# Kernel optimization log

Measured on AMD Instinct MI355X. Metric: run time of the kernel, lower is better.

Reference implementation:

```python
import jax, jax.numpy as jnp
import numpy as np

HID, H, D, DFF = 128, 4, 128, 2048   # hidden_dim, nheads, out_feats per head, dim_feedforward
N, E, B = 32768, 524288, 32
EPS = 1e-5
SLOPE = 0.2  # DGL EdgeGATConv negative_slope default


def setup_inputs() -> dict:
    key = jax.random.key(0)
    ks = jax.random.split(key, 16)
    s = 0.05
    return {
        "h": jax.random.normal(ks[0], (N, HID), jnp.float32),
        "e": jax.random.normal(ks[1], (E, 1), jnp.float32),
        "src": jax.random.randint(ks[2], (E,), 0, N, jnp.int32),
        "dst": jax.random.randint(ks[3], (E,), 0, N, jnp.int32),
        "batch_size": B,
        # EdgeGATConv params (fc / fc_edge / res_fc are bias-free in DGL)
        "W_fc": jax.random.normal(ks[4], (HID, H * D), jnp.float32) * s,
        "attn_l": jax.random.normal(ks[5], (H, D), jnp.float32) * s,
        "attn_r": jax.random.normal(ks[6], (H, D), jnp.float32) * s,
        "W_fe": jax.random.normal(ks[7], (1, H * D), jnp.float32) * s,
        "attn_e": jax.random.normal(ks[8], (H, D), jnp.float32) * s,
        "W_res": jax.random.normal(ks[9], (HID, H * D), jnp.float32) * s,
        "gat_bias": jnp.zeros((H * D,), jnp.float32),
        # linear_mha + norms + FFN
        "W_mha": jax.random.normal(ks[10], (H * D, HID), jnp.float32) * s,
        "b_mha": jnp.zeros((HID,), jnp.float32),
        "n1_g": jnp.ones((HID,), jnp.float32),
        "n1_b": jnp.zeros((HID,), jnp.float32),
        "n2_g": jnp.ones((HID,), jnp.float32),
        "n2_b": jnp.zeros((HID,), jnp.float32),
        "W1": jax.random.normal(ks[11], (HID, DFF), jnp.float32) * s,
        "b1": jnp.zeros((DFF,), jnp.float32),
        "W2": jax.random.normal(ks[12], (DFF, HID), jnp.float32) * s,
        "b2": jnp.zeros((HID,), jnp.float32),
    }


def _ln(x, g, b):
    mu = x.mean(-1, keepdims=True)
    var = ((x - mu) ** 2).mean(-1, keepdims=True)
    return (x - mu) * jax.lax.rsqrt(var + EPS) * g + b


def reference(h, e, src, dst, batch_size, W_fc, attn_l, attn_r, W_fe, attn_e,
              W_res, gat_bias, W_mha, b_mha, n1_g, n1_b, n2_g, n2_b,
              W1, b1, W2, b2):
    n = h.shape[0]
    h0 = h
    # --- EdgeGATConv (eval mode: dropouts are identity) ---
    ft = (h @ W_fc).reshape(n, H, D)                         # (N,H,D)
    el = jnp.einsum("nhd,hd->nh", ft, attn_l)                # (N,H)
    er = jnp.einsum("nhd,hd->nh", ft, attn_r)
    fe = (e @ W_fe).reshape(-1, H, D)                        # (E,H,D)
    ee = jnp.einsum("ehd,hd->eh", fe, attn_e)                # (E,H)
    sc = jax.nn.leaky_relu(el[src] + er[dst] + ee, SLOPE)    # (E,H)
    # segment softmax over incoming edges of each dst node
    m = jax.ops.segment_max(sc, dst, num_segments=n)         # (N,H)
    m = jnp.where(jnp.isfinite(m), m, 0.0)                   # empty segments
    w = jnp.exp(sc - m[dst])
    z = jax.ops.segment_sum(w, dst, num_segments=n)
    zd = z[dst]
    alpha = w / jnp.where(zd == 0, 1.0, zd)                  # (E,H)
    msg = ft[src] * alpha[:, :, None]                        # (E,H,D)
    rst = jax.ops.segment_sum(msg, dst, num_segments=n)      # (N,H,D)
    rst = rst + (h0 @ W_res).reshape(n, H, D) + gat_bias.reshape(1, H, D)
    # --- transformer wrapper ---
    x = jax.nn.relu(rst).reshape(n, H * D)
    x = jax.nn.relu(x @ W_mha + b_mha)
    x = _ln(h0 + x, n1_g, n1_b)
    x = x.reshape(batch_size, -1, x.shape[1])                # (B, N/B, HID)
    ff = jax.nn.relu(x @ W1 + b1) @ W2 + b2
    return _ln(x + ff, n2_g, n2_b)
```

## Files before the change

### kernel.cpp

```cpp
#include <hip/hip_runtime.h>
#include <hip/hip_bf16.h>
#include <hip/hip_fp16.h>

#define N_NODES 32768
#define E_EDGES 524288
#define HIDDIM 128
#define FDIM 512
#define DFF 2048
#define LN_EPS 1e-5f
#define SLOPE 0.2f
#define CAP 64

typedef __bf16 bf16_t;
typedef __bf16 bf16x8 __attribute__((ext_vector_type(8)));
typedef float f32x4 __attribute__((ext_vector_type(4)));
typedef float f32x2 __attribute__((ext_vector_type(2)));

#define GLD_LDS16(gp, lp) __builtin_amdgcn_global_load_lds( \
    (const __attribute__((address_space(1))) unsigned int*)(gp), \
    (__attribute__((address_space(3))) unsigned int*)(lp), 16, 0, 0)

__device__ inline unsigned char f32_to_e4m3(float v) {
#if __has_builtin(__builtin_amdgcn_cvt_pk_fp8_f32)
    return (unsigned char)(__builtin_amdgcn_cvt_pk_fp8_f32(v, v, 0, false) & 0xff);
#else
    unsigned bits = __float_as_uint(v);
    unsigned sign = (bits >> 24) & 0x80;
    float av = fabsf(v);
    if (av >= 448.f) return (unsigned char)(sign | 0x7E);
    int e = (int)((bits >> 23) & 0xFF) - 127;
    if (e < -6) { int n = (int)rintf(av * 512.f); return (unsigned char)(sign | n); }
    float ulp = exp2f((float)(e - 3));
    int n = (int)rintf(av / ulp);
    if (n == 16) { e += 1; n = 8; }
    return (unsigned char)(sign | ((e + 7) << 3) | (n - 8));
#endif
}
template<bool HI>
__device__ inline f32x2 e4m3x2_to_f32(unsigned u) {
#if __has_builtin(__builtin_amdgcn_cvt_pk_f32_fp8)
    return __builtin_amdgcn_cvt_pk_f32_fp8(u, HI);
#else
    f32x2 r;
    unsigned b0 = HI ? ((u >> 16) & 0xff) : (u & 0xff);
    unsigned b1 = HI ? ((u >> 24) & 0xff) : ((u >> 8) & 0xff);
    unsigned bs[2] = {b0, b1};
    for (int i = 0; i < 2; ++i) {
        unsigned b = bs[i];
        float s = (b & 0x80) ? -1.f : 1.f;
        int e = (b >> 3) & 15, m = b & 7;
        float v = e ? (8 + m) * exp2f((float)(e - 10)) : m * exp2f(-9.f);
        r[i] = s * v;
    }
    return r;
#endif
}

__device__ inline void pack_range(const float* __restrict__ B, bf16_t* __restrict__ out,
                                  int id, int N) {
    const int g = id / N, n = id % N;
    union { bf16_t b[8]; uint4 u; } pk;
#pragma unroll
    for (int j = 0; j < 8; ++j) pk.b[j] = (bf16_t)B[(size_t)(g * 8 + j) * N + n];
    *(uint4*)(out + (size_t)id * 8) = pk.u;
}

__global__ __launch_bounds__(256) void prep_kernel(const float* __restrict__ h, bf16_t* __restrict__ hb,
                                                   const float* __restrict__ W_fc, bf16_t* __restrict__ Wfc_p,
                                                   const float* __restrict__ W_res, bf16_t* __restrict__ Wres_p,
                                                   const float* __restrict__ W_mha, bf16_t* __restrict__ Wmha_p,
                                                   const float* __restrict__ W1, bf16_t* __restrict__ W1_p,
                                                   const float* __restrict__ W2, bf16_t* __restrict__ W2_p,
                                                   const float* __restrict__ W_fe, const float* __restrict__ attn_e,
                                                   float* __restrict__ ce) {
    int bid = blockIdx.x;
    const int tid = threadIdx.x;
    if (bid < 4096) {
        const int id = bid * 256 + tid;
        const float4 v = ((const float4*)h)[id];
        union { bf16_t b[4]; uint2 u; } pk;
        pk.b[0] = (bf16_t)v.x; pk.b[1] = (bf16_t)v.y; pk.b[2] = (bf16_t)v.z; pk.b[3] = (bf16_t)v.w;
        *(uint2*)(hb + (size_t)id * 4) = pk.u;
        return;
    }
    bid -= 4096;
    if (bid < 32)  { pack_range(W_fc,  Wfc_p,  bid * 256 + tid, 512);  return; }
    bid -= 32;
    if (bid < 32)  { pack_range(W_res, Wres_p, bid * 256 + tid, 512);  return; }
    bid -= 32;
    if (bid < 32)  { pack_range(W_mha, Wmha_p, bid * 256 + tid, 128);  return; }
    bid -= 32;
    if (bid < 128) { pack_range(W1,    W1_p,   bid * 256 + tid, 2048); return; }
    bid -= 128;
    if (bid < 128) { pack_range(W2,    W2_p,   bid * 256 + tid, 128);  return; }
    if (tid < 128) {
        const float4 w = ((const float4*)W_fe)[tid];
        const float4 a = ((const float4*)attn_e)[tid];
        float p = w.x * a.x + w.y * a.y + w.z * a.z + w.w * a.w;
        for (int off = 16; off; off >>= 1) p += __shfl_down(p, off, 32);
        if ((tid & 31) == 0) ce[tid >> 5] = p;
    }
}

__global__ __launch_bounds__(256, 2) void gemm_ftres(const bf16_t* __restrict__ A,
                                                     const bf16_t* __restrict__ Bf,
                                                     const bf16_t* __restrict__ Brs,
                                                     const float* __restrict__ attn_l,
                                                     const float* __restrict__ attn_r,
                                                     unsigned char* __restrict__ ft8,
                                                     float* __restrict__ el,
                                                     float* __restrict__ er,
                                                     bf16_t* __restrict__ res) {
    __shared__ __align__(16) bf16_t lA[4096];
    __shared__ __align__(16) bf16_t lBf[4096];
    __shared__ __align__(16) bf16_t lBr[4096];
    __shared__ float s_el[2][128], s_er[2][128];
    const int tid = threadIdx.x, lane = tid & 63, wave = tid >> 6;
    const int wm = (wave >> 1) * 64, wn = (wave & 1) * 64;
    const int row0 = blockIdx.y * 128;
    const int head = blockIdx.x, col0 = head * 128;
    const int ko = lane >> 4, rl = lane & 15;
    f32x4 accf[4][4] = {};
    f32x4 accr[4][4] = {};
    const int c0 = tid, c1 = tid + 256;
    const int g0 = c0 >> 7, m0 = c0 & 127;
    const int g1 = c1 >> 7, m1 = c1 & 127;
    for (int k0 = 0; k0 < 128; k0 += 32) {
        __syncthreads();
        GLD_LDS16(A + (size_t)(row0 + m0) * 128 + k0 + g0 * 8, lA + c0 * 8);
        GLD_LDS16(A + (size_t)(row0 + m1) * 128 + k0 + g1 * 8, lA + c1 * 8);
        GLD_LDS16(Bf + ((size_t)(k0 / 8 + g0) * 512 + col0 + m0) * 8, lBf + c0 * 8);
        GLD_LDS16(Bf + ((size_t)(k0 / 8 + g1) * 512 + col0 + m1) * 8, lBf + c1 * 8);
        GLD_LDS16(Brs + ((size_t)(k0 / 8 + g0) * 512 + col0 + m0) * 8, lBr + c0 * 8);
        GLD_LDS16(Brs + ((size_t)(k0 / 8 + g1) * 512 + col0 + m1) * 8, lBr + c1 * 8);
        __syncthreads();
        bf16x8 af[4], bff[4], bfr[4];
#pragma unroll
        for (int i = 0; i < 4; ++i) {
            af[i]  = *(const bf16x8*)&lA[(ko * 128 + wm + i * 16 + rl) * 8];
            bff[i] = *(const bf16x8*)&lBf[(ko * 128 + wn + i * 16 + rl) * 8];
            bfr[i] = *(const bf16x8*)&lBr[(ko * 128 + wn + i * 16 + rl) * 8];
        }
#pragma unroll
        for (int i = 0; i < 4; ++i)
#pragma unroll
            for (int j = 0; j < 4; ++j) {
                accf[i][j] = __builtin_amdgcn_mfma_f32_16x16x32_bf16(af[i], bff[j], accf[i][j], 0, 0, 0);
                accr[i][j] = __builtin_amdgcn_mfma_f32_16x16x32_bf16(af[i], bfr[j], accr[i][j], 0, 0, 0);
            }
    }
    const int cr = (lane >> 4) * 4, cc = lane & 15;
    float al[4], ar[4];
#pragma unroll
    for (int j = 0; j < 4; ++j) {
        al[j] = attn_l[col0 + wn + j * 16 + cc];
        ar[j] = attn_r[col0 + wn + j * 16 + cc];
    }
#pragma unroll
    for (int i = 0; i < 4; ++i)
#pragma unroll
        for (int r = 0; r < 4; ++r) {
            const int row = row0 + wm + i * 16 + cr + r;
            float pel = 0.f, per = 0.f;
#pragma unroll
            for (int j = 0; j < 4; ++j) {
                const int col = col0 + wn + j * 16 + cc;
                const float v = accf[i][j][r];
                ft8[(size_t)row * 512 + col] = f32_to_e4m3(v);
                res[(size_t)row * 512 + col] = (bf16_t)accr[i][j][r];
                pel += v * al[j];
                per += v * ar[j];
            }
#pragma unroll
            for (int m = 1; m < 16; m <<= 1) {
                pel += __shfl_xor(pel, m);
                per += __shfl_xor(per, m);
            }
            if (cc == 0) {
                s_el[wn >> 6][wm + i * 16 + cr + r] = pel;
                s_er[wn >> 6][wm + i * 16 + cr + r] = per;
            }
        }
    __syncthreads();
    if (tid < 128) {
        el[(size_t)(row0 + tid) * 4 + head] = s_el[0][tid] + s_el[1][tid];
        er[(size_t)(row0 + tid) * 4 + head] = s_er[0][tid] + s_er[1][tid];
    }
}

__global__ __launch_bounds__(512, 2) void ffn_mega(const bf16_t* __restrict__ x1,
                                                   const bf16_t* __restrict__ Wm,
                                                   const float* __restrict__ b_mha,
                                                   const float* __restrict__ h0,
                                                   const float* __restrict__ n1g,
                                                   const float* __restrict__ n1b,
                                                   bf16_t* __restrict__ x3stash,
                                                   const bf16_t* __restrict__ W1p,
                                                   const float* __restrict__ b1,
                                                   const bf16_t* __restrict__ W2p,
                                                   const float* __restrict__ b2,
                                                   const float* __restrict__ gamma,
                                                   const float* __restrict__ beta,
                                                   float* __restrict__ out) {
    __shared__ __align__(16) bf16_t lW1[3][8192];
    __shared__ __align__(16) bf16_t lW2[4][8192];
    __shared__ __align__(16) bf16_t lY[2][8192];
    __shared__ float s_s1[2][128], s_s2[2][128], s_mu[128], s_rs[128];
    const int tid = threadIdx.x, lane = tid & 63, wave = tid >> 6;
    const int kh  = wave & 1;
    const int ds  = wave & 3;
    const int cg  = (wave >> 1) & 1;
    const int rg  = wave >> 2;
    const int wr  = rg * 64;
    const int wc1 = ds * 16;
    const int wc2 = cg * 64;
    const int row0 = blockIdx.x * 128;
    const int ko = lane >> 4, rl = lane & 15;
    const int cr = ko * 4, cc = rl;

    {
        const int rg2 = wave >> 1;
        const int cg2 = wave & 1;
        bf16_t* lA = &lY[0][0];
        bf16_t* lB = &lY[0][4096];
        f32x4 am[2][4] = {};
        for (int k0 = 0; k0 < 512; k0 += 32) {
            __syncthreads();
            {
                const int g = tid >> 7, m = tid & 127;
                GLD_LDS16(x1 + (size_t)(row0 + m) * 512 + k0 + g * 8, lA + tid * 8);
                GLD_LDS16(Wm + ((size_t)(k0 / 8 + g) * 128 + m) * 8, lB + tid * 8);
            }
            __syncthreads();
            bf16x8 af[2], bf[4];
#pragma unroll
            for (int i = 0; i < 2; ++i)
                af[i] = *(const bf16x8*)&lA[(ko * 128 + rg2 * 32 + i * 16 + rl) * 8];
#pragma unroll
            for (int j = 0; j < 4; ++j)
                bf[j] = *(const bf16x8*)&lB[(ko * 128 + cg2 * 64 + j * 16 + rl) * 8];
#pragma unroll
            for (int i = 0; i < 2; ++i)
#pragma unroll
                for (int j = 0; j < 4; ++j)
                    am[i][j] = __builtin_amdgcn_mfma_f32_16x16x32_bf16(af[i], bf[j], am[i][j], 0, 0, 0);
        }
#pragma unroll
        for (int j = 0; j < 4; ++j) {
            const int col = cg2 * 64 + j * 16 + cc;
            const float bb = b_mha[col];
#pragma unroll
            for (int i = 0; i < 2; ++i)
#pragma unroll
                for (int r = 0; r < 4; ++r) {
                    const int row = row0 + rg2 * 32 + i * 16 + cr + r;
                    am[i][j][r] = fmaxf(am[i][j][r] + bb, 0.f) + h0[(size_t)row * 128 + col];
                }
        }
#pragma unroll
        for (int i = 0; i < 2; ++i)
#pragma unroll
            for (int r = 0; r < 4; ++r) {
                float s1 = 0.f, s2 = 0.f;
#pragma unroll
                for (int j = 0; j < 4; ++j) { const float v = am[i][j][r]; s1 += v; s2 += v * v; }
#pragma unroll
                for (int m = 1; m < 16; m <<= 1) {
                    s1 += __shfl_xor(s1, m);
                    s2 += __shfl_xor(s2, m);
                }
                if (cc == 0) {
                    s_s1[cg2][rg2 * 32 + i * 16 + cr + r] = s1;
                    s_s2[cg2][rg2 * 32 + i * 16 + cr + r] = s2;
                }
            }
        __syncthreads();
        if (tid < 128) {
            const float a = s_s1[0][tid] + s_s1[1][tid];
            const float q = s_s2[0][tid] + s_s2[1][tid];
            const float mu = a * (1.f / 128.f);
            s_mu[tid] = mu;
            s_rs[tid] = rsqrtf(q * (1.f / 128.f) - mu * mu + LN_EPS);
        }
        __syncthreads();
        bf16_t* lX0 = &lW1[0][0];
#pragma unroll
        for (int j = 0; j < 4; ++j) {
            const int col = cg2 * 64 + j * 16 + cc;
            const float gg = n1g[col], bbta = n1b[col];
#pragma unroll
            for (int i = 0; i < 2; ++i)
#pragma unroll
                for (int r = 0; r < 4; ++r) {
                    const int rloc = rg2 * 32 + i * 16 + cr + r;
                    const bf16_t v = (bf16_t)((am[i][j][r] - s_mu[rloc]) * s_rs[rloc] * gg + bbta);
                    lX0[((col >> 3) * 128 + rloc) * 8 + (col & 7)] = v;
                    x3stash[(size_t)(row0 + rloc) * 128 + col] = v;
                }
        }
    }
    __syncthreads();

    bf16_t* lX = &lW1[0][0];
    bf16x8 afx[4][4];
#pragma unroll
    for (int ir = 0; ir < 4; ++ir)
#pragma unroll
        for (int kk = 0; kk < 4; ++kk)
            afx[ir][kk] = *(const bf16x8*)&lX[((kk * 4 + ko) * 128 + wr + ir * 16 + rl) * 8];
    asm volatile("s_waitcnt lgkmcnt(0)" ::: "memory");
    __builtin_amdgcn_s_barrier();
    __builtin_amdgcn_sched_barrier(0);

    auto stage_chunk = [&](int chn, bf16_t* w1d, bf16_t* w2d) {
#pragma unroll
        for (int it = 0; it < 2; ++it) {
            const int c = it * 512 + tid, g = c >> 6, n = c & 63;
            GLD_LDS16(W1p + ((size_t)g * 2048 + chn * 64 + n) * 8, w1d + c * 8);
        }
#pragma unroll
        for (int it = 0; it < 2; ++it) {
            const int c = it * 512 + tid, g = c >> 7, n = c & 127;
            GLD_LDS16(W2p + ((size_t)(chn * 8 + g) * 128 + n) * 8, w2d + c * 8);
        }
    };

    f32x4 xacc[4][4] = {};

    auto gemm1 = [&](int chn, const bf16_t* w1c, bf16_t* ydst) {
        f32x4 yacc[4] = {};
        __builtin_amdgcn_s_setprio(1);
#pragma unroll
        for (int kk = 0; kk < 4; ++kk) {
            const bf16x8 bw = *(const bf16x8*)&w1c[((kk * 4 + ko) * 64 + wc1 + rl) * 8];
#pragma unroll
            for (int ir = 0; ir < 4; ++ir)
                yacc[ir] = __builtin_amdgcn_mfma_f32_16x16x32_bf16(bw, afx[ir][kk], yacc[ir], 0, 0, 0);
        }
        __builtin_amdgcn_s_setprio(0);
        const int dffb = wc1 + cr;
        const float4 bb = *(const float4*)(b1 + chn * 64 + dffb);
#pragma unroll
        for (int ir = 0; ir < 4; ++ir) {
            const int rowx = wr + ir * 16 + cc;
            union { bf16_t b[4]; uint2 u; } pk;
            pk.b[0] = (bf16_t)fmaxf(yacc[ir][0] + bb.x, 0.f);
            pk.b[1] = (bf16_t)fmaxf(yacc[ir][1] + bb.y, 0.f);
            pk.b[2] = (bf16_t)fmaxf(yacc[ir][2] + bb.z, 0.f);
            pk.b[3] = (bf16_t)fmaxf(yacc[ir][3] + bb.w, 0.f);
            *(uint2*)&ydst[((dffb >> 3) * 128 + rowx) * 8 + (dffb & 7)] = pk.u;
        }
    };

    auto gemm2 = [&](const bf16_t* w2c, const bf16_t* ysrc) {
        bf16x8 ay[4], bw2[4];
#pragma unroll
        for (int ir = 0; ir < 4; ++ir)
            ay[ir] = *(const bf16x8*)&ysrc[((kh * 4 + ko) * 128 + wr + ir * 16 + rl) * 8];
#pragma unroll
        for (int j = 0; j < 4; ++j)
            bw2[j] = *(const bf16x8*)&w2c[((kh * 4 + ko) * 128 + wc2 + j * 16 + rl) * 8];
        __builtin_amdgcn_s_setprio(1);
#pragma unroll
        for (int ir = 0; ir < 4; ++ir)
#pragma unroll
            for (int j = 0; j < 4; ++j)
                xacc[ir][j] = __builtin_amdgcn_mfma_f32_16x16x32_bf16(ay[ir], bw2[j], xacc[ir][j], 0, 0, 0);
        __builtin_amdgcn_s_setprio(0);
    };

#pragma unroll
    for (int pc = 0; pc < 2; ++pc)
        stage_chunk(pc, lW1[pc], lW2[pc]);
    asm volatile("s_waitcnt vmcnt(4)" ::: "memory");
    __builtin_amdgcn_s_barrier();
    __builtin_amdgcn_sched_barrier(0);

    stage_chunk(2, lW1[2], lW2[2]);
    gemm1(0, lW1[0], lY[0]);
    __builtin_amdgcn_sched_barrier(0);
    asm volatile("s_waitcnt vmcnt(4) lgkmcnt(0)" ::: "memory");
    __builtin_amdgcn_s_barrier();
    __builtin_amdgcn_sched_barrier(0);

    int r1 = 1, sb1 = 0, r2 = 0, sb2 = 3, p = 1;
#pragma unroll 1
    for (int i = 1; i < 32; ++i) {
        if (i < 30)
            stage_chunk(i + 2, lW1[sb1], lW2[sb2]);
        gemm1(i, lW1[r1], lY[p]);
        gemm2(lW2[r2], lY[p ^ 1]);
        __builtin_amdgcn_sched_barrier(0);
        if (i < 30)
            asm volatile("s_waitcnt vmcnt(4) lgkmcnt(0)" ::: "memory");
        else if (i == 30)
            asm volatile("s_waitcnt vmcnt(2) lgkmcnt(0)" ::: "memory");
        else
            asm volatile("s_waitcnt vmcnt(0) lgkmcnt(0)" ::: "memory");
        __builtin_amdgcn_s_barrier();
        __builtin_amdgcn_sched_barrier(0);
        r1 = (r1 == 2) ? 0 : r1 + 1;
        sb1 = (sb1 == 2) ? 0 : sb1 + 1;
        r2 = (r2 == 3) ? 0 : r2 + 1;
        sb2 = (sb2 == 3) ? 0 : sb2 + 1;
        p ^= 1;
    }
    gemm2(lW2[3], lY[1]);

    __syncthreads();
    {
        const int q = (wave >> 1) & 3;
        float* scr = (q < 2) ? ((float*)&lW1[0][0] + q * 4352)
                             : ((float*)&lW2[0][0] + (q - 2) * 4352);
        if (kh) {
#pragma unroll
            for (int ir = 0; ir < 4; ++ir)
#pragma unroll
                for (int j = 0; j < 4; ++j)
                    *(f32x4*)(scr + lane * 68 + (ir * 4 + j) * 4) = xacc[ir][j];
        }
        __syncthreads();
        if (!kh) {
#pragma unroll
            for (int ir = 0; ir < 4; ++ir)
#pragma unroll
                for (int j = 0; j < 4; ++j)
                    xacc[ir][j] += *(const f32x4*)(scr + lane * 68 + (ir * 4 + j) * 4);
        }
    }

    if (!kh) {
#pragma unroll
        for (int j = 0; j < 4; ++j) {
            const int col = wc2 + j * 16 + cc;
            const float bb = b2[col];
#pragma unroll
            for (int ir = 0; ir < 4; ++ir)
#pragma unroll
                for (int r = 0; r < 4; ++r) {
                    const int row = wr + ir * 16 + cr + r;
                    xacc[ir][j][r] += bb + (float)x3stash[(size_t)(row0 + row) * 128 + col];
                }
        }
#pragma unroll
        for (int ir = 0; ir < 4; ++ir)
#pragma unroll
            for (int r = 0; r < 4; ++r) {
                float s1v = 0.f, s2v = 0.f;
#pragma unroll
                for (int j = 0; j < 4; ++j) { const float v = xacc[ir][j][r]; s1v += v; s2v += v * v; }
#pragma unroll
                for (int m = 1; m < 16; m <<= 1) {
                    s1v += __shfl_xor(s1v, m);
                    s2v += __shfl_xor(s2v, m);
                }
                if (cc == 0) {
                    s_s1[cg][wr + ir * 16 + cr + r] = s1v;
                    s_s2[cg][wr + ir * 16 + cr + r] = s2v;
                }
            }
    }
    __syncthreads();
    if (tid < 128) {
        const float a = s_s1[0][tid] + s_s1[1][tid];
        const float q = s_s2[0][tid] + s_s2[1][tid];
        const float mu = a * (1.f / 128.f);
        s_mu[tid] = mu;
        s_rs[tid] = rsqrtf(q * (1.f / 128.f) - mu * mu + LN_EPS);
    }
    __syncthreads();
    if (!kh) {
#pragma unroll
        for (int j = 0; j < 4; ++j) {
            const int col = wc2 + j * 16 + cc;
            const float gg = gamma[col], bb = beta[col];
#pragma unroll
            for (int ir = 0; ir < 4; ++ir)
#pragma unroll
                for (int r = 0; r < 4; ++r) {
                    const int rloc = wr + ir * 16 + cr + r;
                    out[(size_t)(row0 + rloc) * 128 + col] =
                        (xacc[ir][j][r] - s_mu[rloc]) * s_rs[rloc] * gg + bb;
                }
        }
    }
}

__global__ __launch_bounds__(256) void edge_build(const float* __restrict__ evals,
                                                  const int* __restrict__ src,
                                                  const int* __restrict__ dst,
                                                  const float* __restrict__ el,
                                                  const float* __restrict__ er,
                                                  const float* __restrict__ ce,
                                                  int* __restrict__ cursor,
                                                  uint4* __restrict__ csr) {
    const int e = blockIdx.x * 256 + threadIdx.x;
    const int s = src[e], d = dst[e];
    const float ev = evals[e];
    const float4 l = *(const float4*)(el + (size_t)s * 4);
    const float4 r = *(const float4*)(er + (size_t)d * 4);
    const float4 c = *(const float4*)ce;
    float4 w;
    {
        float v;
        v = l.x + r.x + ev * c.x; v = v >= 0.f ? v : SLOPE * v; w.x = __expf(v);
        v = l.y + r.y + ev * c.y; v = v >= 0.f ? v : SLOPE * v; w.y = __expf(v);
        v = l.z + r.z + ev * c.z; v = v >= 0.f ? v : SLOPE * v; w.z = __expf(v);
        v = l.w + r.w + ev * c.w; v = v >= 0.f ? v : SLOPE * v; w.w = __expf(v);
    }
    const int pos = atomicAdd(&cursor[d], 1);
    if (pos < CAP) {
        uint4 rec;
        rec.x = (unsigned)__half_as_ushort(__float2half(w.x)) |
                ((unsigned)__half_as_ushort(__float2half(w.y)) << 16);
        rec.y = (unsigned)__half_as_ushort(__float2half(w.z)) |
                ((unsigned)__half_as_ushort(__float2half(w.w)) << 16);
        rec.z = (unsigned)s;
        rec.w = 0u;
        csr[(size_t)d * CAP + pos] = rec;
    }
}

__device__ inline float w_of(const uint4& rec, int ht) {
    const unsigned pair = (ht < 2) ? rec.x : rec.y;
    const unsigned sh = (ht & 1) ? (pair >> 16) : (pair & 0xffffu);
    return __half2float(__ushort_as_half((unsigned short)sh));
}

__global__ __launch_bounds__(128) void aggregate_kernel(const unsigned char* __restrict__ ft8,
                                                        const bf16_t* __restrict__ res,
                                                        const int* __restrict__ cursor,
                                                        const uint4* __restrict__ csr,
                                                        const float* __restrict__ gat_bias,
                                                        bf16_t* __restrict__ x1) {
    const int n = blockIdx.x, t = threadIdx.x;
    __shared__ uint4 s_rec[CAP];
    const int deg = min(cursor[n], CAP);
    const int ht = t >> 5;
    if (t < deg) s_rec[t] = csr[(size_t)n * CAP + t];
    __syncthreads();
    float4 acc = {0.f, 0.f, 0.f, 0.f};
    float z = 0.f;
    int j = 0;
    for (; j + 8 <= deg; j += 8) {
        unsigned u[8];
        float w[8];
#pragma unroll
        for (int q = 0; q < 8; ++q) {
            const uint4 rc = s_rec[j + q];
            w[q] = w_of(rc, ht);
            u[q] = *(const unsigned*)(ft8 + (size_t)rc.z * 512 + t * 4);
        }
#pragma unroll
        for (int q = 0; q < 8; ++q) {
            z += w[q];
            const f32x2 lo = e4m3x2_to_f32<false>(u[q]), hi = e4m3x2_to_f32<true>(u[q]);
            acc.x += w[q] * lo[0]; acc.y += w[q] * lo[1];
            acc.z += w[q] * hi[0]; acc.w += w[q] * hi[1];
        }
    }
    for (; j < deg; ++j) {
        const uint4 rc = s_rec[j];
        const float w = w_of(rc, ht);
        z += w;
        const unsigned u = *(const unsigned*)(ft8 + (size_t)rc.z * 512 + t * 4);
        const f32x2 lo = e4m3x2_to_f32<false>(u);
        const f32x2 hi = e4m3x2_to_f32<true>(u);
        acc.x += w * lo[0]; acc.y += w * lo[1];
        acc.z += w * hi[0]; acc.w += w * hi[1];
    }
    const float rz = deg > 0 ? 1.f / z : 0.f;
    const uint2 ur = *(const uint2*)(res + (size_t)n * FDIM + t * 4);
    const float4 gb = ((const float4*)gat_bias)[t];
    union { bf16_t b[4]; uint2 u; } pk;
    pk.b[0] = (bf16_t)fmaxf(acc.x * rz + __uint_as_float(ur.x << 16) + gb.x, 0.f);
    pk.b[1] = (bf16_t)fmaxf(acc.y * rz + __uint_as_float(ur.x & 0xFFFF0000u) + gb.y, 0.f);
    pk.b[2] = (bf16_t)fmaxf(acc.z * rz + __uint_as_float(ur.y << 16) + gb.z, 0.f);
    pk.b[3] = (bf16_t)fmaxf(acc.w * rz + __uint_as_float(ur.y & 0xFFFF0000u) + gb.w, 0.f);
    *(uint2*)(x1 + (size_t)n * FDIM + t * 4) = pk.u;
}

extern "C" void kernel_launch(void* const* d_in, const int* in_sizes, int n_in,
                              void* d_out, int out_size, void* d_ws, size_t ws_size,
                              hipStream_t stream) {
    const float* h        = (const float*)d_in[0];
    const float* evals    = (const float*)d_in[1];
    const int*   src      = (const int*)d_in[2];
    const int*   dst      = (const int*)d_in[3];
    const float* W_fc     = (const float*)d_in[5];
    const float* attn_l   = (const float*)d_in[6];
    const float* attn_r   = (const float*)d_in[7];
    const float* W_fe     = (const float*)d_in[8];
    const float* attn_e   = (const float*)d_in[9];
    const float* W_res    = (const float*)d_in[10];
    const float* gat_bias = (const float*)d_in[11];
    const float* W_mha    = (const float*)d_in[12];
    const float* b_mha    = (const float*)d_in[13];
    const float* n1_g     = (const float*)d_in[14];
    const float* n1_b     = (const float*)d_in[15];
    const float* n2_g     = (const float*)d_in[16];
    const float* n2_b     = (const float*)d_in[17];
    const float* W1       = (const float*)d_in[18];
    const float* b1       = (const float*)d_in[19];
    const float* W2       = (const float*)d_in[20];
    const float* b2       = (const float*)d_in[21];

    char* ws = (char*)d_ws;
    unsigned char* ft8 = (unsigned char*)(ws + 0);
    bf16_t* res     = (bf16_t*)(ws + 16777216ull);
    bf16_t* x1      = (bf16_t*)(ws + 50331648ull);
    uint4*  csr     = (uint4*) (ws + 83886080ull);
    bf16_t* x3b     = (bf16_t*)(ws + 125829120ull);
    bf16_t* hb      = (bf16_t*)(ws + 134217728ull);
    bf16_t* Wfc_p   = (bf16_t*)(ws + 142606336ull);
    bf16_t* Wres_p  = (bf16_t*)(ws + 142737408ull);
    bf16_t* Wmha_p  = (bf16_t*)(ws + 142868480ull);
    bf16_t* W1_p    = (bf16_t*)(ws + 142999552ull);
    bf16_t* W2_p    = (bf16_t*)(ws + 143523840ull);
    float*  el      = (float*) (ws + 144048128ull);
    float*  er      = (float*) (ws + 144572416ull);
    float*  ce      = (float*) (ws + 145096704ull);
    int*    cursor  = (int*)   (ws + 145096768ull);

    if (ws_size < 146000000ull) return;

    (void)hipMemsetAsync(cursor, 0, 131072, stream);

    prep_kernel<<<4449, 256, 0, stream>>>(h, hb, W_fc, Wfc_p, W_res, Wres_p,
                                          W_mha, Wmha_p, W1, W1_p, W2, W2_p,
                                          W_fe, attn_e, ce);
    gemm_ftres<<<dim3(4, 256), 256, 0, stream>>>(hb, Wfc_p, Wres_p, attn_l, attn_r, ft8, el, er, res);
    edge_build<<<E_EDGES / 256, 256, 0, stream>>>(evals, src, dst, el, er, ce, cursor, csr);
    aggregate_kernel<<<N_NODES, 128, 0, stream>>>(ft8, res, cursor, csr, gat_bias, x1);
    ffn_mega<<<256, 512, 0, stream>>>(x1, Wmha_p, b_mha, h, n1_g, n1_b, x3b,
                                      W1_p, b1, W2_p, b2, n2_g, n2_b, (float*)d_out);
}
```

Measured before the change: 283.2 us.

## Pipeline linear_mha K-loop with 4-stage LDS buffers and keep LN1 output in registers

The linear_mha GEMM prologue in ffn_mega now stages x1 and W_mha tiles into a four-deep ring of LDS buffers, three stages ahead. It waits on vmcnt counts with one barrier per step instead of two __syncthreads around each synchronous load, and raises wave priority around the MFMAs. The LN1 output is no longer written to and reread from a global stash. Each wave packs its residual values from LDS into 32 registers, which removes global traffic at the cost of register pressure in a kernel launched with (512,2) bounds.

```diff
diff --git a/kernel.cpp b/kernel.cpp
--- a/kernel.cpp
+++ b/kernel.cpp
@@ -194,7 +194,6 @@
                                                    const float* __restrict__ h0,
                                                    const float* __restrict__ n1g,
                                                    const float* __restrict__ n1b,
-                                                   bf16_t* __restrict__ x3stash,
                                                    const bf16_t* __restrict__ W1p,
                                                    const float* __restrict__ b1,
                                                    const bf16_t* __restrict__ W2p,
@@ -221,29 +220,37 @@
     {
         const int rg2 = wave >> 1;
         const int cg2 = wave & 1;
-        bf16_t* lA = &lY[0][0];
-        bf16_t* lB = &lY[0][4096];
+        const int gg = tid >> 7, mm = tid & 127;
+        auto stage0 = [&](int s) {
+            bf16_t* lab = &lW2[s & 3][0];
+            GLD_LDS16(x1 + (size_t)(row0 + mm) * 512 + s * 32 + gg * 8, lab + tid * 8);
+            GLD_LDS16(Wm + ((size_t)(s * 4 + gg) * 128 + mm) * 8, lab + 4096 + tid * 8);
+        };
         f32x4 am[2][4] = {};
-        for (int k0 = 0; k0 < 512; k0 += 32) {
-            __syncthreads();
-            {
-                const int g = tid >> 7, m = tid & 127;
-                GLD_LDS16(x1 + (size_t)(row0 + m) * 512 + k0 + g * 8, lA + tid * 8);
-                GLD_LDS16(Wm + ((size_t)(k0 / 8 + g) * 128 + m) * 8, lB + tid * 8);
-            }
-            __syncthreads();
-            bf16x8 af[2], bf[4];
+        stage0(0); stage0(1); stage0(2);
+        for (int s = 0; s < 16; ++s) {
+            __builtin_amdgcn_sched_barrier(0);
+            if (s < 14)       asm volatile("s_waitcnt vmcnt(4)" ::: "memory");
+            else if (s == 14) asm volatile("s_waitcnt vmcnt(2)" ::: "memory");
+            else              asm volatile("s_waitcnt vmcnt(0)" ::: "memory");
+            __builtin_amdgcn_s_barrier();
+            __builtin_amdgcn_sched_barrier(0);
+            if (s + 3 < 16) stage0(s + 3);
+            const bf16_t* lab = &lW2[s & 3][0];
+            bf16x8 af[2], bfm[4];
 #pragma unroll
             for (int i = 0; i < 2; ++i)
-                af[i] = *(const bf16x8*)&lA[(ko * 128 + rg2 * 32 + i * 16 + rl) * 8];
+                af[i] = *(const bf16x8*)&lab[(ko * 128 + rg2 * 32 + i * 16 + rl) * 8];
 #pragma unroll
             for (int j = 0; j < 4; ++j)
-                bf[j] = *(const bf16x8*)&lB[(ko * 128 + cg2 * 64 + j * 16 + rl) * 8];
+                bfm[j] = *(const bf16x8*)&lab[4096 + (ko * 128 + cg2 * 64 + j * 16 + rl) * 8];
+            __builtin_amdgcn_s_setprio(1);
 #pragma unroll
             for (int i = 0; i < 2; ++i)
 #pragma unroll
                 for (int j = 0; j < 4; ++j)
-                    am[i][j] = __builtin_amdgcn_mfma_f32_16x16x32_bf16(af[i], bf[j], am[i][j], 0, 0, 0);
+                    am[i][j] = __builtin_amdgcn_mfma_f32_16x16x32_bf16(af[i], bfm[j], am[i][j], 0, 0, 0);
+            __builtin_amdgcn_s_setprio(0);
         }
 #pragma unroll
         for (int j = 0; j < 4; ++j) {
@@ -287,15 +294,14 @@
 #pragma unroll
         for (int j = 0; j < 4; ++j) {
             const int col = cg2 * 64 + j * 16 + cc;
-            const float gg = n1g[col], bbta = n1b[col];
+            const float gg2 = n1g[col], bbta = n1b[col];
 #pragma unroll
             for (int i = 0; i < 2; ++i)
 #pragma unroll
                 for (int r = 0; r < 4; ++r) {
                     const int rloc = rg2 * 32 + i * 16 + cr + r;
-                    const bf16_t v = (bf16_t)((am[i][j][r] - s_mu[rloc]) * s_rs[rloc] * gg + bbta);
-                    lX0[((col >> 3) * 128 + rloc) * 8 + (col & 7)] = v;
-                    x3stash[(size_t)(row0 + rloc) * 128 + col] = v;
+                    lX0[((col >> 3) * 128 + rloc) * 8 + (col & 7)] =
+                        (bf16_t)((am[i][j][r] - s_mu[rloc]) * s_rs[rloc] * gg2 + bbta);
                 }
         }
     }
@@ -308,6 +314,21 @@
 #pragma unroll
         for (int kk = 0; kk < 4; ++kk)
             afx[ir][kk] = *(const bf16x8*)&lX[((kk * 4 + ko) * 128 + wr + ir * 16 + rl) * 8];
+    unsigned x3p[32];
+    if (!kh) {
+#pragma unroll
+        for (int ir = 0; ir < 4; ++ir)
+#pragma unroll
+            for (int j = 0; j < 4; ++j)
+#pragma unroll
+                for (int rr = 0; rr < 2; ++rr) {
+                    const int col = wc2 + j * 16 + cc;
+                    const int rw = wr + ir * 16 + cr + rr * 2;
+                    const unsigned short a = *(const unsigned short*)&lX[((col >> 3) * 128 + rw) * 8 + (col & 7)];
+                    const unsigned short b = *(const unsigned short*)&lX[((col >> 3) * 128 + rw + 1) * 8 + (col & 7)];
+                    x3p[ir * 8 + j * 2 + rr] = (unsigned)a | ((unsigned)b << 16);
+                }
+    }
     asm volatile("s_waitcnt lgkmcnt(0)" ::: "memory");
     __builtin_amdgcn_s_barrier();
     __builtin_amdgcn_sched_barrier(0);
@@ -438,8 +459,9 @@
             for (int ir = 0; ir < 4; ++ir)
 #pragma unroll
                 for (int r = 0; r < 4; ++r) {
-                    const int row = wr + ir * 16 + cr + r;
-                    xacc[ir][j][r] += bb + (float)x3stash[(size_t)(row0 + row) * 128 + col];
+                    const unsigned dw = x3p[ir * 8 + j * 2 + (r >> 1)];
+                    const float xv = __uint_as_float((r & 1) ? (dw & 0xFFFF0000u) : (dw << 16));
+                    xacc[ir][j][r] += bb + xv;
                 }
         }
 #pragma unroll
@@ -610,7 +632,6 @@
     bf16_t* res     = (bf16_t*)(ws + 16777216ull);
     bf16_t* x1      = (bf16_t*)(ws + 50331648ull);
     uint4*  csr     = (uint4*) (ws + 83886080ull);
-    bf16_t* x3b     = (bf16_t*)(ws + 125829120ull);
     bf16_t* hb      = (bf16_t*)(ws + 134217728ull);
     bf16_t* Wfc_p   = (bf16_t*)(ws + 142606336ull);
     bf16_t* Wres_p  = (bf16_t*)(ws + 142737408ull);
@@ -632,6 +653,6 @@
     gemm_ftres<<<dim3(4, 256), 256, 0, stream>>>(hb, Wfc_p, Wres_p, attn_l, attn_r, ft8, el, er, res);
     edge_build<<<E_EDGES / 256, 256, 0, stream>>>(evals, src, dst, el, er, ce, cursor, csr);
     aggregate_kernel<<<N_NODES, 128, 0, stream>>>(ft8, res, cursor, csr, gat_bias, x1);
-    ffn_mega<<<256, 512, 0, stream>>>(x1, Wmha_p, b_mha, h, n1_g, n1_b, x3b,
+    ffn_mega<<<256, 512, 0, stream>>>(x1, Wmha_p, b_mha, h, n1_g, n1_b,
                                       W1_p, b1, W2_p, b2, n2_g, n2_b, (float*)d_out);
 }
```

Result: faster. 270.9 us (-4.3%).
